# Kernel optimization log

Hardware: AMD Instinct MI355X
Metric: run time of the kernel (lower is better)

Reference implementation:

```python
import jax, jax.numpy as jnp
import numpy as np

N_VIEWS = 4
VIEW_DIM = 48
N_CLASSES = 16
D = VIEW_DIM ** N_VIEWS  # 5,308,416 cross-feature dims


def setup_inputs() -> dict:
    key = jax.random.key(0)
    kx, kw = jax.random.split(key)
    x = jax.random.normal(kx, (N_VIEWS, VIEW_DIM), dtype=jnp.float32)
    # pyg Linear(-1, n_classes): kaiming_uniform weight (scale ~ 1/sqrt(fan_in)), zero bias
    W = jax.random.normal(kw, (N_CLASSES, D), dtype=jnp.float32) * np.float32(1.0 / np.sqrt(D))
    b = jnp.zeros((N_CLASSES,), dtype=jnp.float32)
    return {"x": x, "W": W, "b": b}


def _cross_feature_tensor(x):
    # Faithful to construct_cross_feature_discovery_tensor:
    # outer(x0, x1) -> flatten -> outer(., x2) -> flatten -> ...
    # Loop is over the fixed, small n_views axis (static under jit).
    t = jnp.outer(x[0], x[1]).ravel()          # (VIEW_DIM**2,)
    for v in x[2:]:
        t = jnp.outer(t, v).ravel()            # grows to VIEW_DIM**k
    return t                                   # (D,)


def reference(x, W, b):
    cfdt = _cross_feature_tensor(x)            # (D,)
    return jax.nn.relu(W @ cfdt + b)           # (N_CLASSES,)
```

## Files before the change

kernel.cpp:

```cpp
#include <hip/hip_runtime.h>


#define N_CLASSES 16
#define VIEW_DIM  48
#define P         2304
#define ROW_F4    (P / 4)
#define ROWS_PER_BLOCK 24
#define CHUNKS    (P / ROWS_PER_BLOCK)
#define ROWS_PER_WAVE  6
#define BLOCK     256
#define ITERS     (ROW_F4 / 64)

typedef float v4f __attribute__((ext_vector_type(4)));

__global__ __launch_bounds__(BLOCK, 6) void vcdn_main(
        const float* __restrict__ x,
        const float* __restrict__ W,
        float* __restrict__ ws) {
    __shared__ float p23[P];

    const float* x0 = x;
    const float* x1 = x + VIEW_DIM;
    const float* x2 = x + 2 * VIEW_DIM;
    const float* x3 = x + 3 * VIEW_DIM;

    for (int t = threadIdx.x; t < P; t += BLOCK) {
        int i = t / VIEW_DIM;
        int j = t - i * VIEW_DIM;
        p23[t] = x2[i] * x3[j];
    }
    __syncthreads();

    const int c     = blockIdx.x / CHUNKS;
    const int chunk = blockIdx.x - c * CHUNKS;
    const int wid   = threadIdx.x >> 6;
    const int lane  = threadIdx.x & 63;

    const v4f* q4 = (const v4f*)p23;
    v4f q[ITERS];
#pragma unroll
    for (int it = 0; it < ITERS; ++it) q[it] = q4[it * 64 + lane];

    const int row0 = chunk * ROWS_PER_BLOCK + wid * ROWS_PER_WAVE;
    float acc0 = 0.0f, acc1 = 0.0f;

#pragma unroll
    for (int r = 0; r < ROWS_PER_WAVE; ++r) {
        const int a = row0 + r;
        const int i = a / VIEW_DIM;
        const int j = a - i * VIEW_DIM;
        const float s01 = x0[i] * x1[j];

        const v4f* Wrow =
            (const v4f*)(W + (size_t)c * (size_t)P * P + (size_t)a * P);

        float racc = 0.0f;
#pragma unroll
        for (int it = 0; it < ITERS; ++it) {
            v4f w = __builtin_nontemporal_load(Wrow + it * 64 + lane);
            racc += w.x * q[it].x + w.y * q[it].y + w.z * q[it].z + w.w * q[it].w;
        }
        if (r & 1) acc1 += s01 * racc;
        else       acc0 += s01 * racc;
    }
    float acc = acc0 + acc1;

    for (int off = 32; off; off >>= 1)
        acc += __shfl_down(acc, off, 64);

    __shared__ float wsum[BLOCK / 64];
    if (lane == 0) wsum[wid] = acc;
    __syncthreads();
    if (threadIdx.x == 0)
        ws[c * CHUNKS + chunk] = wsum[0] + wsum[1] + wsum[2] + wsum[3];
}

__global__ void vcdn_finalize(const float* __restrict__ ws,
                              const float* __restrict__ b,
                              float* __restrict__ out) {
    __shared__ float s[BLOCK];
    const int t   = threadIdx.x;
    const int c   = t >> 4;
    const int sub = t & 15;
    float sum = 0.0f;
    for (int k = sub; k < CHUNKS; k += 16)
        sum += ws[c * CHUNKS + k];
    s[t] = sum;
    __syncthreads();
    if (t < N_CLASSES) {
        float tot = 0.0f;
#pragma unroll
        for (int k = 0; k < 16; ++k) tot += s[t * 16 + k];
        tot += b[t];
        out[t] = tot > 0.0f ? tot : 0.0f;
    }
}

extern "C" void kernel_launch(void* const* d_in, const int* in_sizes, int n_in,
                              void* d_out, int out_size, void* d_ws, size_t ws_size,
                              hipStream_t stream) {
    const float* x = (const float*)d_in[0];
    const float* W = (const float*)d_in[1];
    const float* b = (const float*)d_in[2];
    float* out = (float*)d_out;
    float* ws  = (float*)d_ws;

    vcdn_main<<<N_CLASSES * CHUNKS, BLOCK, 0, stream>>>(x, W, ws);
    vcdn_finalize<<<1, BLOCK, 0, stream>>>(ws, b, out);
}
```

Baseline: 417.7 us.

## Stream W through per-wave LDS ring via global_load_lds with manual vmcnt pipelining

Replaces the direct nontemporal register loads of W with a per-wave 6-deep LDS ring buffer filled by global_load_lds (direct-to-LDS DMA), with explicit s_waitcnt vmcnt counters so several 1 KiB chunks per wave stay in flight. The x2*x3 outer product is now computed in registers per lane instead of staged through shared memory, which removes the initial block barrier. The goal is a deeper, steadier memory pipeline for this bandwidth-bound GEMV. The cost is an extra LDS round trip per chunk and a tight lgkmcnt wait before each re-issue, and the pipelining relies on exact hand-written wait counts.

```diff
diff --git a/kernel.cpp b/kernel.cpp
--- a/kernel.cpp
+++ b/kernel.cpp
@@ -4,71 +4,102 @@
 #define N_CLASSES 16
 #define VIEW_DIM  48
 #define P         2304
-#define ROW_F4    (P / 4)
 #define ROWS_PER_BLOCK 24
 #define CHUNKS    (P / ROWS_PER_BLOCK)
 #define ROWS_PER_WAVE  6
 #define BLOCK     256
-#define ITERS     (ROW_F4 / 64)
+#define NWAVES    4
+#define CPR       9
+#define TOTC      (ROWS_PER_WAVE * CPR)
+#define DEPTH     6
 
 typedef float v4f __attribute__((ext_vector_type(4)));
+
+__device__ __forceinline__ void stage1k(const float* gsrc, float* lds_uniform) {
+    __builtin_amdgcn_global_load_lds(
+        (const __attribute__((address_space(1))) unsigned int*)gsrc,
+        (__attribute__((address_space(3))) unsigned int*)lds_uniform,
+        16, 0, 0);
+}
 
 __global__ __launch_bounds__(BLOCK, 6) void vcdn_main(
         const float* __restrict__ x,
         const float* __restrict__ W,
         float* __restrict__ ws) {
-    __shared__ float p23[P];
+    __shared__ float ring[NWAVES][DEPTH][256];
+
+    const int c     = blockIdx.x / CHUNKS;
+    const int chunk = blockIdx.x - c * CHUNKS;
+    const int wid   = threadIdx.x >> 6;
+    const int lane  = threadIdx.x & 63;
 
     const float* x0 = x;
     const float* x1 = x + VIEW_DIM;
     const float* x2 = x + 2 * VIEW_DIM;
     const float* x3 = x + 3 * VIEW_DIM;
 
-    for (int t = threadIdx.x; t < P; t += BLOCK) {
-        int i = t / VIEW_DIM;
-        int j = t - i * VIEW_DIM;
-        p23[t] = x2[i] * x3[j];
+    const int row0 = chunk * ROWS_PER_BLOCK + wid * ROWS_PER_WAVE;
+
+    v4f q[CPR];
+#pragma unroll
+    for (int k = 0; k < CPR; ++k) {
+#pragma unroll
+        for (int e = 0; e < 4; ++e) {
+            const int t = k * 256 + lane * 4 + e;
+            const int i = t / VIEW_DIM;
+            const int j = t - i * VIEW_DIM;
+            q[k][e] = x2[i] * x3[j];
+        }
     }
-    __syncthreads();
 
-    const int c     = blockIdx.x / CHUNKS;
-    const int chunk = blockIdx.x - c * CHUNKS;
-    const int wid   = threadIdx.x >> 6;
-    const int lane  = threadIdx.x & 63;
-
-    const v4f* q4 = (const v4f*)p23;
-    v4f q[ITERS];
-#pragma unroll
-    for (int it = 0; it < ITERS; ++it) q[it] = q4[it * 64 + lane];
-
-    const int row0 = chunk * ROWS_PER_BLOCK + wid * ROWS_PER_WAVE;
-    float acc0 = 0.0f, acc1 = 0.0f;
-
+    float s01[ROWS_PER_WAVE];
 #pragma unroll
     for (int r = 0; r < ROWS_PER_WAVE; ++r) {
         const int a = row0 + r;
         const int i = a / VIEW_DIM;
         const int j = a - i * VIEW_DIM;
-        const float s01 = x0[i] * x1[j];
+        s01[r] = x0[i] * x1[j];
+    }
 
-        const v4f* Wrow =
-            (const v4f*)(W + (size_t)c * (size_t)P * P + (size_t)a * P);
+    const float* wbase = W + (size_t)c * (size_t)(P * P) + (size_t)row0 * P;
+    float* myring = &ring[wid][0][0];
 
+    asm volatile("s_waitcnt vmcnt(0)" ::: "memory");
+
+#pragma unroll
+    for (int m = 0; m < DEPTH; ++m)
+        stage1k(wbase + m * 256 + lane * 4, myring + m * 256);
+
+    float acc = 0.0f;
+#pragma unroll
+    for (int r = 0; r < ROWS_PER_WAVE; ++r) {
         float racc = 0.0f;
 #pragma unroll
-        for (int it = 0; it < ITERS; ++it) {
-            v4f w = __builtin_nontemporal_load(Wrow + it * 64 + lane);
-            racc += w.x * q[it].x + w.y * q[it].y + w.z * q[it].z + w.w * q[it].w;
+        for (int k = 0; k < CPR; ++k) {
+            const int m    = r * CPR + k;
+            const int slot = m % DEPTH;
+            const int wn = (TOTC - 1 - m) < (DEPTH - 1) ? (TOTC - 1 - m) : (DEPTH - 1);
+            switch (wn) {
+                case 0: asm volatile("s_waitcnt vmcnt(0)" ::: "memory"); break;
+                case 1: asm volatile("s_waitcnt vmcnt(1)" ::: "memory"); break;
+                case 2: asm volatile("s_waitcnt vmcnt(2)" ::: "memory"); break;
+                case 3: asm volatile("s_waitcnt vmcnt(3)" ::: "memory"); break;
+                case 4: asm volatile("s_waitcnt vmcnt(4)" ::: "memory"); break;
+                default: asm volatile("s_waitcnt vmcnt(5)" ::: "memory"); break;
+            }
+            v4f w = *(const v4f*)(myring + slot * 256 + lane * 4);
+            asm volatile("s_waitcnt lgkmcnt(0)" ::: "memory");
+            if (m < TOTC - DEPTH)
+                stage1k(wbase + (m + DEPTH) * 256 + lane * 4, myring + slot * 256);
+            racc += w.x * q[k].x + w.y * q[k].y + w.z * q[k].z + w.w * q[k].w;
         }
-        if (r & 1) acc1 += s01 * racc;
-        else       acc0 += s01 * racc;
+        acc += s01[r] * racc;
     }
-    float acc = acc0 + acc1;
 
     for (int off = 32; off; off >>= 1)
         acc += __shfl_down(acc, off, 64);
 
-    __shared__ float wsum[BLOCK / 64];
+    __shared__ float wsum[NWAVES];
     if (lane == 0) wsum[wid] = acc;
     __syncthreads();
     if (threadIdx.x == 0)
```

New measurement: 448.4 us. 7.4% more time.
